# Kernel tuning notes

Measured on AMD Instinct MI355X. Metric: run time of the kernel, lower is better.

## Reference

```python
import jax, jax.numpy as jnp
import numpy as np

N_NODES = 100000
N_EDGES = 1600000
D = 128


def setup_inputs() -> dict:
    key = jax.random.key(0)
    ks = jax.random.split(key, 6)
    x = jax.random.normal(ks[0], (N_NODES, D), dtype=jnp.float32)
    src = jax.random.randint(ks[1], (N_EDGES,), 0, N_NODES, dtype=jnp.int32)
    dst = jax.random.randint(ks[2], (N_EDGES,), 0, N_NODES, dtype=jnp.int32)
    # Xavier-ish small weights
    W1 = jax.random.normal(ks[3], (D, D), dtype=jnp.float32) * 0.05
    W2 = jax.random.normal(ks[4], (D, D), dtype=jnp.float32) * 0.05
    b1 = jnp.zeros((D,), dtype=jnp.float32)
    b2 = jnp.zeros((D,), dtype=jnp.float32)
    prelu_a = jnp.full((1,), 0.25, dtype=jnp.float32)  # nn.PReLU default, shared across layers
    return {"x": x, "src": src, "dst": dst, "W1": W1, "b1": b1, "W2": W2, "b2": b2, "prelu_a": prelu_a}


def reference(x, src, dst, W1, b1, W2, b2, prelu_a):
    N = x.shape[0]
    # DGL GraphConv norm='left': scale source features by 1/clamp(out_degree, 1)
    deg = jax.ops.segment_sum(jnp.ones(src.shape, x.dtype), src, num_segments=N)
    inv_outdeg = (1.0 / jnp.maximum(deg, 1.0))[:, None]  # [N,1]

    def layer(h, W, b):
        h = h * inv_outdeg                                   # left-normalize sources
        agg = jax.ops.segment_sum(h[src], dst, num_segments=N)  # SpMM: sum messages at dst
        z = agg @ W + b                                      # dense transform (aggregate-first since in==out feats)
        return jnp.where(z >= 0, z, prelu_a * z)             # shared PReLU

    z = layer(x, W1, b1)
    z = layer(z, W2, b2)
    return z
```

## Files before the change

### kernel.cpp

```cpp
#include <hip/hip_runtime.h>

#define D 128
#define CAP 64
#define PADR 136

#define BSHIFT 9
#define NCH 512
#define BSTRIDE_LOG 14

typedef short short8 __attribute__((ext_vector_type(8)));
typedef float floatx4 __attribute__((ext_vector_type(4)));

static __device__ __forceinline__ unsigned short f2bf(float f) {
    unsigned int u = __float_as_uint(f);
    u += 0x7fffu + ((u >> 16) & 1u);
    return (unsigned short)(u >> 16);
}
static __device__ __forceinline__ unsigned int pack2bf(float a, float b) {
    return (unsigned int)f2bf(a) | ((unsigned int)f2bf(b) << 16);
}
static __device__ __forceinline__ int rd16(const unsigned int* __restrict__ pc, int v) {
    return (int)((pc[v >> 1] >> ((v & 1) * 16)) & 0xffffu);
}
static __device__ __forceinline__ void acc8(float* a, uint4 v) {
    a[0] += __uint_as_float(v.x << 16);  a[1] += __uint_as_float(v.x & 0xffff0000u);
    a[2] += __uint_as_float(v.y << 16);  a[3] += __uint_as_float(v.y & 0xffff0000u);
    a[4] += __uint_as_float(v.z << 16);  a[5] += __uint_as_float(v.z & 0xffff0000u);
    a[6] += __uint_as_float(v.w << 16);  a[7] += __uint_as_float(v.w & 0xffff0000u);
}

__global__ __launch_bounds__(512) void k_cnt(const int* __restrict__ src,
                                             const int* __restrict__ dst,
                                             unsigned int* __restrict__ gcnt,
                                             unsigned int* __restrict__ pcnt_out,
                                             int E, int cs, int nbuck) {
    __shared__ unsigned int h[512];
    int b = blockIdx.x, t = threadIdx.x;
    for (int k = t; k < nbuck; k += 512) h[k] = 0;
    __syncthreads();
    int lo = b * cs, hi = lo + cs;
    if (hi > E) hi = E;
    for (int e = lo + t; e < hi; e += 512) {
        atomicAdd(&h[(unsigned)dst[e] >> BSHIFT], 1u);
        int s = src[e];
        atomicAdd(&pcnt_out[s >> 1], 1u << ((s & 1) * 16));
    }
    __syncthreads();
    for (int k = t; k < nbuck; k += 512) gcnt[(size_t)b * nbuck + k] = h[k];
}

__global__ __launch_bounds__(NCH) void k_pfx1(unsigned int* __restrict__ gcnt,
                                              unsigned int* __restrict__ btot, int nbuck) {
    __shared__ unsigned int sa[NCH], sb[NCH];
    int k = blockIdx.x, t = threadIdx.x;
    unsigned int v = gcnt[(size_t)t * nbuck + k];
    sa[t] = v;
    unsigned int* A = sa; unsigned int* B = sb;
    for (int off = 1; off < NCH; off <<= 1) {
        __syncthreads();
        B[t] = A[t] + ((t >= off) ? A[t - off] : 0u);
        unsigned int* tmp = A; A = B; B = tmp;
    }
    __syncthreads();
    unsigned int incl = A[t];
    gcnt[(size_t)t * nbuck + k] = incl - v;
    if (t == NCH - 1) btot[k] = incl;
}

__global__ __launch_bounds__(512) void k_scat(const int* __restrict__ src, const int* __restrict__ dst,
                                              const unsigned int* __restrict__ goff,
                                              unsigned int* __restrict__ bdata,
                                              int E, int cs, int nbuck) {
    __shared__ unsigned int cur[512];
    int b = blockIdx.x, t = threadIdx.x;
    for (int k = t; k < nbuck; k += 512)
        cur[k] = ((unsigned int)k << BSTRIDE_LOG) + goff[(size_t)b * nbuck + k];
    __syncthreads();
    int lo = b * cs, hi = lo + cs;
    if (hi > E) hi = E;
    for (int e = lo + t; e < hi; e += 512) {
        int s = src[e];
        int d = dst[e];
        unsigned int kb = (unsigned)d >> BSHIFT;
        unsigned int p = atomicAdd(&cur[kb], 1u);
        if (p < ((kb + 1u) << BSTRIDE_LOG))
            bdata[p] = ((unsigned int)(d & ((1 << BSHIFT) - 1)) << 17) | (unsigned int)s;
    }
}

__global__ __launch_bounds__(256) void k_csrprep(
    const unsigned int* __restrict__ bdata, const unsigned int* __restrict__ btot,
    unsigned int* __restrict__ pcnt_in, int* __restrict__ esrc,
    const float* __restrict__ x, const unsigned int* __restrict__ pcnt_out,
    float* __restrict__ inv, uint2* __restrict__ xb2, int total4,
    const float* __restrict__ W1, const float* __restrict__ W2,
    unsigned short* __restrict__ WT1, unsigned short* __restrict__ WT2,
    uint4* __restrict__ z0, uint4* __restrict__ z1,
    int n, int nbuck) {
    __shared__ unsigned int lcnt[1 << BSHIFT];
    int b = blockIdx.x;

    if (b < nbuck) {
        int base = b << BSHIFT;
        for (int k = threadIdx.x; k < (1 << BSHIFT); k += 256) lcnt[k] = 0;
        __syncthreads();
        int lo = b << BSTRIDE_LOG;
        int cnt = (int)btot[b];
        if (cnt > (1 << BSTRIDE_LOG)) cnt = 1 << BSTRIDE_LOG;
        for (int i = threadIdx.x; i < cnt; i += 256) {
            unsigned int e = bdata[lo + i];
            int s = (int)(e & 0x1FFFFu);
            int dl = (int)(e >> 17);
            unsigned int p = atomicAdd(&lcnt[dl], 1u);
            if (p < CAP) esrc[((size_t)(base + dl) << 6) + p] = s;
        }
        __syncthreads();
        for (int nn = threadIdx.x; nn < (1 << BSHIFT); nn += 256) {
            int node = base + nn;
            if (node < n) {
                int c = (int)lcnt[nn];
                if (c > CAP) c = CAP;
                int cp = (c + 7) & ~7;
                for (int p = c; p < cp; p++)
                    esrc[((size_t)node << 6) + p] = n;
            }
        }
        for (int tt = threadIdx.x; tt < (1 << (BSHIFT - 1)); tt += 256) {
            int node0 = base + tt * 2;
            if (node0 < n) {
                unsigned int c0 = lcnt[tt * 2];
                unsigned int c1 = lcnt[tt * 2 + 1];
                pcnt_in[(base >> 1) + tt] = (c0 & 0xffffu) | (c1 << 16);
            }
        }
        return;
    }

    int bb = b - nbuck;
    int nb4 = (total4 + 255) >> 8;
    if (bb >= nb4 + 128) {
        if (threadIdx.x < 16) z0[threadIdx.x] = (uint4){0u, 0u, 0u, 0u};
        else if (threadIdx.x < 32) z1[threadIdx.x - 16] = (uint4){0u, 0u, 0u, 0u};
        return;
    }
    if (bb >= nb4) {
        int wb = bb - nb4;
        const float* W = (wb < 64) ? W1 : W2;
        unsigned short* WT = (wb < 64) ? WT1 : WT2;
        int idx = (wb & 63) * 256 + threadIdx.x;
        int k = idx >> 7, nn = idx & 127;
        WT[nn * 128 + k] = f2bf(W[idx]);
        return;
    }
    int i = bb * 256 + threadIdx.x;
    if (i >= total4) return;
    int row = i >> 5;
    int d = rd16(pcnt_out, row);
    float s = 1.0f / (float)(d > 1 ? d : 1);
    if ((i & 31) == 0) inv[row] = s;
    float4 v = ((const float4*)x)[i];
    uint2 o;
    o.x = pack2bf(v.x * s, v.y * s);
    o.y = pack2bf(v.z * s, v.w * s);
    xb2[i] = o;
}

template<bool OUTBF>
__global__ __launch_bounds__(256) void k_fused(
    const uint4* __restrict__ hb4, const unsigned int* __restrict__ pcnt_in,
    const int* __restrict__ esrc, const unsigned short* __restrict__ WT,
    const float* __restrict__ bias, const float* __restrict__ pa,
    const float* __restrict__ inv, void* __restrict__ outp, int n)
{
    __shared__ unsigned short sAgg[16 * PADR];
    int wv = threadIdx.x >> 6;
    int lane = threadIdx.x & 63;
    int q = lane >> 4;
    int f = lane & 15;
    int nb = blockIdx.x * 16;

    for (int ii = 0; ii < 4; ii += 2) {
        int nodeA = nb + wv * 4 + ii;
        int nodeB = nodeA + 1;
        int cA = (nodeA < n) ? rd16(pcnt_in, nodeA) : 0;
        int cB = (nodeB < n) ? rd16(pcnt_in, nodeB) : 0;
        if (cA > CAP) cA = CAP;
        if (cB > CAP) cB = CAP;
        cA = (cA + 7) & ~7;
        cB = (cB + 7) & ~7;
        const int* epA = esrc + ((size_t)nodeA << 6);
        const int* epB = esrc + ((size_t)nodeB << 6);
        float accA[8], accB[8];
#pragma unroll
        for (int j = 0; j < 8; j++) { accA[j] = 0.f; accB[j] = 0.f; }
        int mx = cA > cB ? cA : cB;
        for (int base = 0; base < mx; base += 8) {
            bool dA = base < cA, dB = base < cB;
            int2 eA, eB;
            uint4 vA0, vA1, vB0, vB1;
            if (dA) eA = *(const int2*)(epA + base + 2 * q);
            if (dB) eB = *(const int2*)(epB + base + 2 * q);
            if (dA) { vA0 = hb4[(size_t)eA.x * 16 + f]; vA1 = hb4[(size_t)eA.y * 16 + f]; }
            if (dB) { vB0 = hb4[(size_t)eB.x * 16 + f]; vB1 = hb4[(size_t)eB.y * 16 + f]; }
            if (dA) { acc8(accA, vA0); acc8(accA, vA1); }
            if (dB) { acc8(accB, vB0); acc8(accB, vB1); }
        }
#pragma unroll
        for (int j = 0; j < 8; j++) {
            accA[j] += __shfl_xor(accA[j], 16, 64);
            accA[j] += __shfl_xor(accA[j], 32, 64);
            accB[j] += __shfl_xor(accB[j], 16, 64);
            accB[j] += __shfl_xor(accB[j], 32, 64);
        }
        if (q == 0) {
            uint4 oA, oB;
            oA.x = pack2bf(accA[0], accA[1]); oA.y = pack2bf(accA[2], accA[3]);
            oA.z = pack2bf(accA[4], accA[5]); oA.w = pack2bf(accA[6], accA[7]);
            oB.x = pack2bf(accB[0], accB[1]); oB.y = pack2bf(accB[2], accB[3]);
            oB.z = pack2bf(accB[4], accB[5]); oB.w = pack2bf(accB[6], accB[7]);
            if (nodeA < n) *(uint4*)&sAgg[(wv * 4 + ii) * PADR + f * 8] = oA;
            if (nodeB < n) *(uint4*)&sAgg[(wv * 4 + ii + 1) * PADR + f * 8] = oB;
        }
    }
    __syncthreads();

    int m = lane & 15;
    short8 a0 = *(const short8*)&sAgg[m * PADR +   0 + q * 8];
    short8 a1 = *(const short8*)&sAgg[m * PADR +  32 + q * 8];
    short8 a2 = *(const short8*)&sAgg[m * PADR +  64 + q * 8];
    short8 a3 = *(const short8*)&sAgg[m * PADR +  96 + q * 8];

    float alpha = pa[0];
    float* outf = (float*)outp;
    unsigned short* outb = (unsigned short*)outp;

    float invr[4];
    if (OUTBF) {
#pragma unroll
        for (int r = 0; r < 4; r++) {
            int row = nb + q * 4 + r;
            invr[r] = (row < n) ? inv[row] : 1.f;
        }
    }

#pragma unroll
    for (int tt = 0; tt < 2; tt++) {
        int t = wv * 2 + tt;
        int col = t * 16 + m;
        const short8* Bp = (const short8*)(WT + (size_t)col * 128 + q * 8);
        floatx4 acc = {0.f, 0.f, 0.f, 0.f};
        acc = __builtin_amdgcn_mfma_f32_16x16x32_bf16(a0, Bp[0],  acc, 0, 0, 0);
        acc = __builtin_amdgcn_mfma_f32_16x16x32_bf16(a1, Bp[4],  acc, 0, 0, 0);
        acc = __builtin_amdgcn_mfma_f32_16x16x32_bf16(a2, Bp[8],  acc, 0, 0, 0);
        acc = __builtin_amdgcn_mfma_f32_16x16x32_bf16(a3, Bp[12], acc, 0, 0, 0);
        float bb = bias[col];
#pragma unroll
        for (int r = 0; r < 4; r++) {
            int row = nb + q * 4 + r;
            if (row < n) {
                float z = acc[r] + bb;
                z = (z >= 0.f) ? z : alpha * z;
                if (OUTBF)
                    outb[(size_t)row * 128 + col] = f2bf(z * invr[r]);
                else
                    __builtin_nontemporal_store(z, &outf[(size_t)row * 128 + col]);
            }
        }
    }
}

__global__ __launch_bounds__(256) void k_gather(
    const uint4* __restrict__ hb4, const unsigned int* __restrict__ pcnt_in,
    const int* __restrict__ esrc, uint4* __restrict__ aggb4, int n)
{
    int lane = threadIdx.x & 63;
    int node = blockIdx.x * 4 + (threadIdx.x >> 6);
    if (node >= n) return;
    int q = lane >> 4, f = lane & 15;
    int cnt = rd16(pcnt_in, node);
    if (cnt > CAP) cnt = CAP;
    cnt = (cnt + 7) & ~7;
    const int* ep = esrc + ((size_t)node << 6);

    float acc[8];
#pragma unroll
    for (int j = 0; j < 8; j++) acc[j] = 0.f;

    for (int base = 0; base < cnt; base += 8) {
        int2 e = *(const int2*)(ep + base + 2 * q);
        uint4 v0 = hb4[(size_t)e.x * 16 + f];
        uint4 v1 = hb4[(size_t)e.y * 16 + f];
        acc8(acc, v0);
        acc8(acc, v1);
    }
#pragma unroll
    for (int j = 0; j < 8; j++) {
        acc[j] += __shfl_xor(acc[j], 16, 64);
        acc[j] += __shfl_xor(acc[j], 32, 64);
    }
    if (q == 0) {
        uint4 o;
        o.x = pack2bf(acc[0], acc[1]);
        o.y = pack2bf(acc[2], acc[3]);
        o.z = pack2bf(acc[4], acc[5]);
        o.w = pack2bf(acc[6], acc[7]);
        aggb4[(size_t)node * 16 + f] = o;
    }
}

__global__ __launch_bounds__(256) void k_gemm(
    const unsigned short* __restrict__ A, const unsigned short* __restrict__ WT,
    const float* __restrict__ bias, const float* __restrict__ pa,
    float* __restrict__ outf, int n)
{
    int lane = threadIdx.x & 63;
    int wv = threadIdx.x >> 6;
    int m = lane & 15, q = lane >> 4;
    int mbase = blockIdx.x * 64 + wv * 16;
    int arow = mbase + m;
    if (arow > n - 1) arow = n - 1;

    const short8* Ap = (const short8*)(A + (size_t)arow * 128 + q * 8);
    short8 a0 = Ap[0], a1 = Ap[4], a2 = Ap[8], a3 = Ap[12];

    float alpha = pa[0];
#pragma unroll
    for (int t = 0; t < 8; t++) {
        int col = t * 16 + m;
        const short8* Bp = (const short8*)(WT + (size_t)col * 128 + q * 8);
        floatx4 acc = {0.f, 0.f, 0.f, 0.f};
        acc = __builtin_amdgcn_mfma_f32_16x16x32_bf16(a0, Bp[0],  acc, 0, 0, 0);
        acc = __builtin_amdgcn_mfma_f32_16x16x32_bf16(a1, Bp[4],  acc, 0, 0, 0);
        acc = __builtin_amdgcn_mfma_f32_16x16x32_bf16(a2, Bp[8],  acc, 0, 0, 0);
        acc = __builtin_amdgcn_mfma_f32_16x16x32_bf16(a3, Bp[12], acc, 0, 0, 0);
        float bb = bias[col];
#pragma unroll
        for (int r = 0; r < 4; r++) {
            int row = mbase + q * 4 + r;
            if (row < n) {
                float z = acc[r] + bb;
                z = (z >= 0.f) ? z : alpha * z;
                outf[(size_t)row * 128 + col] = z;
            }
        }
    }
}

extern "C" void kernel_launch(void* const* d_in, const int* in_sizes, int n_in,
                              void* d_out, int out_size, void* d_ws, size_t ws_size,
                              hipStream_t stream) {
    const float* x   = (const float*)d_in[0];
    const int* src   = (const int*)d_in[1];
    const int* dst   = (const int*)d_in[2];
    const float* W1  = (const float*)d_in[3];
    const float* b1  = (const float*)d_in[4];
    const float* W2  = (const float*)d_in[5];
    const float* b2  = (const float*)d_in[6];
    const float* pa  = (const float*)d_in[7];
    float* out = (float*)d_out;

    const int N = in_sizes[0] / D;
    const int E = in_sizes[1];

    char* ws = (char*)d_ws;
    size_t off = 0;
    unsigned short* buf0 = (unsigned short*)(ws + off); off += (size_t)(N + 1) * D * 2;
    unsigned short* buf1 = (unsigned short*)(ws + off); off += (size_t)(N + 1) * D * 2;
    const size_t pc_words = (size_t)((N + 1) / 2);
    unsigned int* pcnt_out = (unsigned int*)(ws + off); off += pc_words * 4;
    unsigned int* pcnt_in  = (unsigned int*)(ws + off); off += pc_words * 4;
    float* inv   = (float*)(ws + off); off += (size_t)N * sizeof(float);
    unsigned short* WT1 = (unsigned short*)(ws + off); off += 128 * 128 * 2;
    unsigned short* WT2 = (unsigned short*)(ws + off); off += 128 * 128 * 2;
    size_t off_esrc = off;
    size_t need_big = off_esrc + (size_t)N * CAP * sizeof(int);
    bool big = (ws_size >= need_big);

    int* esrc = big ? (int*)(ws + off_esrc) : (int*)d_out;

    const int nbuck = (N + (1 << BSHIFT) - 1) >> BSHIFT;
    unsigned int* bdata  = (unsigned int*)buf1;
    unsigned int* gcnt   = bdata + ((size_t)nbuck << BSTRIDE_LOG);
    unsigned int* btot   = gcnt + (size_t)NCH * nbuck;

    const int cs = (E + NCH - 1) / NCH;
    const int total4 = N * (D / 4);
    uint4* z0 = (uint4*)(buf0 + (size_t)N * D);
    uint4* z1 = (uint4*)(buf1 + (size_t)N * D);

    hipMemsetAsync(pcnt_out, 0, pc_words * 4, stream);

    k_cnt <<<NCH, 512, 0, stream>>>(src, dst, gcnt, pcnt_out, E, cs, nbuck);
    k_pfx1<<<nbuck, NCH, 0, stream>>>(gcnt, btot, nbuck);
    k_scat<<<NCH, 512, 0, stream>>>(src, dst, gcnt, bdata, E, cs, nbuck);

    const int nb4 = (total4 + 255) / 256;
    const int NBC = nbuck + nb4 + 128 + 1;
    k_csrprep<<<NBC, 256, 0, stream>>>(bdata, btot, pcnt_in, esrc,
                                       x, pcnt_out, inv, (uint2*)buf0, total4,
                                       W1, W2, WT1, WT2, z0, z1, N, nbuck);

    const int NBF = (N + 15) / 16;

    k_fused<true><<<NBF, 256, 0, stream>>>((const uint4*)buf0, pcnt_in, esrc, WT1, b1, pa, inv,
                                           (void*)buf1, N);

    if (big) {
        k_fused<false><<<NBF, 256, 0, stream>>>((const uint4*)buf1, pcnt_in, esrc, WT2, b2, pa, inv,
                                                (void*)out, N);
    } else {
        const int NBG = (N + 3) / 4;
        const int NBM = (N + 63) / 64;
        k_gather<<<NBG, 256, 0, stream>>>((const uint4*)buf1, pcnt_in, esrc, (uint4*)buf0, N);
        k_gemm<<<NBM, 256, 0, stream>>>(buf0, WT2, b2, pa, out, N);
    }
}
```

Baseline: 380.7 us.

## Compute out-degrees via bucketed shared-memory histogram instead of global atomics

Replaces the per-edge global atomicAdd on packed 16-bit out-degree counters with a second bucket sort of source IDs: per-block histograms, prefix sums, scatter into bucketed storage, and a new kernel that counts each bucket in shared memory and writes packed counts. This removes the 1.6M contended global atomics and the memset, in exchange for a second scatter pass, extra prefix-scan blocks and one more kernel launch. Source data is scattered into buf0, which is later overwritten by csrprep.

```diff
diff --git a/kernel.cpp b/kernel.cpp
--- a/kernel.cpp
+++ b/kernel.cpp
@@ -31,29 +31,36 @@
 
 __global__ __launch_bounds__(512) void k_cnt(const int* __restrict__ src,
                                              const int* __restrict__ dst,
-                                             unsigned int* __restrict__ gcnt,
-                                             unsigned int* __restrict__ pcnt_out,
+                                             unsigned int* __restrict__ gcd,
+                                             unsigned int* __restrict__ gcs,
                                              int E, int cs, int nbuck) {
-    __shared__ unsigned int h[512];
+    __shared__ unsigned int hd[512], hs[512];
     int b = blockIdx.x, t = threadIdx.x;
-    for (int k = t; k < nbuck; k += 512) h[k] = 0;
+    hd[t] = 0; hs[t] = 0;
     __syncthreads();
     int lo = b * cs, hi = lo + cs;
     if (hi > E) hi = E;
     for (int e = lo + t; e < hi; e += 512) {
-        atomicAdd(&h[(unsigned)dst[e] >> BSHIFT], 1u);
-        int s = src[e];
-        atomicAdd(&pcnt_out[s >> 1], 1u << ((s & 1) * 16));
-    }
-    __syncthreads();
-    for (int k = t; k < nbuck; k += 512) gcnt[(size_t)b * nbuck + k] = h[k];
-}
-
-__global__ __launch_bounds__(NCH) void k_pfx1(unsigned int* __restrict__ gcnt,
-                                              unsigned int* __restrict__ btot, int nbuck) {
+        atomicAdd(&hd[(unsigned)dst[e] >> BSHIFT], 1u);
+        atomicAdd(&hs[(unsigned)src[e] >> BSHIFT], 1u);
+    }
+    __syncthreads();
+    for (int k = t; k < nbuck; k += 512) {
+        gcd[(size_t)b * nbuck + k] = hd[k];
+        gcs[(size_t)b * nbuck + k] = hs[k];
+    }
+}
+
+__global__ __launch_bounds__(NCH) void k_pfx1(unsigned int* __restrict__ gcd,
+                                              unsigned int* __restrict__ gcs,
+                                              unsigned int* __restrict__ btd,
+                                              unsigned int* __restrict__ bts, int nbuck) {
     __shared__ unsigned int sa[NCH], sb[NCH];
-    int k = blockIdx.x, t = threadIdx.x;
-    unsigned int v = gcnt[(size_t)t * nbuck + k];
+    int b = blockIdx.x, t = threadIdx.x;
+    unsigned int* g  = (b < nbuck) ? gcd : gcs;
+    unsigned int* bt = (b < nbuck) ? btd : bts;
+    int k = (b < nbuck) ? b : (b - nbuck);
+    unsigned int v = g[(size_t)t * nbuck + k];
     sa[t] = v;
     unsigned int* A = sa; unsigned int* B = sb;
     for (int off = 1; off < NCH; off <<= 1) {
@@ -63,28 +70,60 @@
     }
     __syncthreads();
     unsigned int incl = A[t];
-    gcnt[(size_t)t * nbuck + k] = incl - v;
-    if (t == NCH - 1) btot[k] = incl;
+    g[(size_t)t * nbuck + k] = incl - v;
+    if (t == NCH - 1) bt[k] = incl;
 }
 
 __global__ __launch_bounds__(512) void k_scat(const int* __restrict__ src, const int* __restrict__ dst,
-                                              const unsigned int* __restrict__ goff,
+                                              const unsigned int* __restrict__ gcd,
+                                              const unsigned int* __restrict__ gcs,
                                               unsigned int* __restrict__ bdata,
+                                              unsigned int* __restrict__ sdata,
                                               int E, int cs, int nbuck) {
-    __shared__ unsigned int cur[512];
+    __shared__ unsigned int curd[512], curs[512];
     int b = blockIdx.x, t = threadIdx.x;
-    for (int k = t; k < nbuck; k += 512)
-        cur[k] = ((unsigned int)k << BSTRIDE_LOG) + goff[(size_t)b * nbuck + k];
+    for (int k = t; k < nbuck; k += 512) {
+        curd[k] = ((unsigned int)k << BSTRIDE_LOG) + gcd[(size_t)b * nbuck + k];
+        curs[k] = ((unsigned int)k << BSTRIDE_LOG) + gcs[(size_t)b * nbuck + k];
+    }
     __syncthreads();
     int lo = b * cs, hi = lo + cs;
     if (hi > E) hi = E;
     for (int e = lo + t; e < hi; e += 512) {
         int s = src[e];
         int d = dst[e];
-        unsigned int kb = (unsigned)d >> BSHIFT;
-        unsigned int p = atomicAdd(&cur[kb], 1u);
-        if (p < ((kb + 1u) << BSTRIDE_LOG))
+        unsigned int kd = (unsigned)d >> BSHIFT;
+        unsigned int p = atomicAdd(&curd[kd], 1u);
+        if (p < ((kd + 1u) << BSTRIDE_LOG))
             bdata[p] = ((unsigned int)(d & ((1 << BSHIFT) - 1)) << 17) | (unsigned int)s;
+        unsigned int ks = (unsigned)s >> BSHIFT;
+        unsigned int p2 = atomicAdd(&curs[ks], 1u);
+        if (p2 < ((ks + 1u) << BSTRIDE_LOG))
+            sdata[p2] = (unsigned int)(s & ((1 << BSHIFT) - 1));
+    }
+}
+
+__global__ __launch_bounds__(256) void k_sdeg(const unsigned int* __restrict__ sdata,
+                                              const unsigned int* __restrict__ bts,
+                                              unsigned int* __restrict__ pcnt_out, int n) {
+    __shared__ unsigned int cnt[1 << BSHIFT];
+    int b = blockIdx.x;
+    for (int k = threadIdx.x; k < (1 << BSHIFT); k += 256) cnt[k] = 0;
+    __syncthreads();
+    int lo = b << BSTRIDE_LOG;
+    int c = (int)bts[b];
+    if (c > (1 << BSTRIDE_LOG)) c = 1 << BSTRIDE_LOG;
+    for (int i = threadIdx.x; i < c; i += 256)
+        atomicAdd(&cnt[sdata[lo + i]], 1u);
+    __syncthreads();
+    int base = b << BSHIFT;
+    for (int tt = threadIdx.x; tt < (1 << (BSHIFT - 1)); tt += 256) {
+        int node0 = base + tt * 2;
+        if (node0 < n) {
+            unsigned int c0 = cnt[tt * 2];
+            unsigned int c1 = cnt[tt * 2 + 1];
+            pcnt_out[(base >> 1) + tt] = (c0 & 0xffffu) | (c1 << 16);
+        }
     }
 }
 
@@ -379,24 +418,26 @@
     int* esrc = big ? (int*)(ws + off_esrc) : (int*)d_out;
 
     const int nbuck = (N + (1 << BSHIFT) - 1) >> BSHIFT;
-    unsigned int* bdata  = (unsigned int*)buf1;
-    unsigned int* gcnt   = bdata + ((size_t)nbuck << BSTRIDE_LOG);
-    unsigned int* btot   = gcnt + (size_t)NCH * nbuck;
+    unsigned int* bdata = (unsigned int*)buf1;
+    unsigned int* gcd   = bdata + ((size_t)nbuck << BSTRIDE_LOG);
+    unsigned int* gcs   = gcd + (size_t)NCH * nbuck;
+    unsigned int* btd   = gcs + (size_t)NCH * nbuck;
+    unsigned int* bts   = btd + nbuck;
+    unsigned int* sdata = (unsigned int*)buf0;
 
     const int cs = (E + NCH - 1) / NCH;
     const int total4 = N * (D / 4);
     uint4* z0 = (uint4*)(buf0 + (size_t)N * D);
     uint4* z1 = (uint4*)(buf1 + (size_t)N * D);
 
-    hipMemsetAsync(pcnt_out, 0, pc_words * 4, stream);
-
-    k_cnt <<<NCH, 512, 0, stream>>>(src, dst, gcnt, pcnt_out, E, cs, nbuck);
-    k_pfx1<<<nbuck, NCH, 0, stream>>>(gcnt, btot, nbuck);
-    k_scat<<<NCH, 512, 0, stream>>>(src, dst, gcnt, bdata, E, cs, nbuck);
+    k_cnt <<<NCH, 512, 0, stream>>>(src, dst, gcd, gcs, E, cs, nbuck);
+    k_pfx1<<<2 * nbuck, NCH, 0, stream>>>(gcd, gcs, btd, bts, nbuck);
+    k_scat<<<NCH, 512, 0, stream>>>(src, dst, gcd, gcs, bdata, sdata, E, cs, nbuck);
+    k_sdeg<<<nbuck, 256, 0, stream>>>(sdata, bts, pcnt_out, N);
 
     const int nb4 = (total4 + 255) / 256;
     const int NBC = nbuck + nb4 + 128 + 1;
-    k_csrprep<<<NBC, 256, 0, stream>>>(bdata, btot, pcnt_in, esrc,
+    k_csrprep<<<NBC, 256, 0, stream>>>(bdata, btd, pcnt_in, esrc,
                                        x, pcnt_out, inv, (uint2*)buf0, total4,
                                        W1, W2, WT1, WT2, z0, z1, N, nbuck);
 
```

New measurement: 336.3 us, median of 2. 1.13x faster.
